# Kernel optimization log

Hardware: AMD Instinct MI355X
Metric: run time of the kernel (lower is better)

The kernel has to match this reference:

```python
import jax, jax.numpy as jnp
import numpy as np

N_NODES = 100000
N_EDGES = 2000000


def _init_mlp(key, dims, scale=0.05):
    Ws, bs = [], []
    ks = jax.random.split(key, len(dims) - 1)
    for k, di, do in zip(ks, dims[:-1], dims[1:]):
        Ws.append(jax.random.normal(k, (di, do), dtype=jnp.float32) * scale)
        bs.append(jnp.zeros((do,), dtype=jnp.float32))
    return Ws, bs


def setup_inputs() -> dict:
    key = jax.random.key(0)
    ks = jax.random.split(key, 7)
    d = {
        "t": jax.random.uniform(ks[0], (1,), dtype=jnp.float32),
        "x": jax.random.normal(ks[1], (N_NODES, 4), dtype=jnp.float32),
        "Ofixed": jax.random.normal(ks[2], (N_NODES, 2), dtype=jnp.float32),
        "src_idx": jax.random.randint(ks[3], (N_EDGES,), 0, N_NODES, dtype=jnp.int32),
        "tgt_idx": jax.random.randint(ks[4], (N_EDGES,), 0, N_NODES, dtype=jnp.int32),
    }
    # fR: (2*d_O+1)=13 -> [150]*4 -> 50 ; fO: 50 -> [100] -> 4
    R_Ws, R_bs = _init_mlp(ks[5], [13, 150, 150, 150, 150, 50])
    O_Ws, O_bs = _init_mlp(ks[6], [50, 100, 4])
    for i, (W, b) in enumerate(zip(R_Ws, R_bs)):
        d[f"fR_W{i}"] = W
        d[f"fR_b{i}"] = b
    for i, (W, b) in enumerate(zip(O_Ws, O_bs)):
        d[f"fO_W{i}"] = W
        d[f"fO_b{i}"] = b
    return d


def _mlp(h, Ws, bs):
    # hidden layers with ReLU, linear output (matches MLP in the torch code)
    for W, b in zip(Ws[:-1], bs[:-1]):
        h = jax.nn.relu(h @ W + b)
    return h @ Ws[-1] + bs[-1]


def reference(t, x, Ofixed, src_idx, tgt_idx,
              fR_W0, fR_b0, fR_W1, fR_b1, fR_W2, fR_b2, fR_W3, fR_b3, fR_W4, fR_b4,
              fO_W0, fO_b0, fO_W1, fO_b1):
    O = jnp.concatenate([x, Ofixed], axis=1)            # [N, d_O]
    # Msrc.T @ O and Mtgt.T @ O with 0/1 incidence matrices == gathers
    Rsrc = O[src_idx]                                   # [M, d_O]
    Rtgt = O[tgt_idx]                                   # [M, d_O]
    tt = jnp.broadcast_to(t.reshape(1, 1).astype(O.dtype), (src_idx.shape[0], 1))
    R_prime = jnp.concatenate([Rsrc, Rtgt, tt], axis=1)  # [M, 2*d_O+1]
    E = _mlp(R_prime, [fR_W0, fR_W1, fR_W2, fR_W3, fR_W4],
             [fR_b0, fR_b1, fR_b2, fR_b3, fR_b4])        # [M, d_E]
    # Mtgt @ E == scatter-add of edge messages onto target nodes
    E_prime = jax.ops.segment_sum(E, tgt_idx, num_segments=x.shape[0])  # [N, d_E]
    P = _mlp(E_prime, [fO_W0, fO_W1], [fO_b0, fO_b1])    # [N, d_P]
    return P
```

## Files before the change

kernel.cpp:

```cpp
#include <hip/hip_runtime.h>
#include <hip/hip_bf16.h>

typedef unsigned short u16;
typedef unsigned int u32;
typedef __attribute__((ext_vector_type(8))) short short8;
typedef __attribute__((ext_vector_type(4))) float f32x4;

constexpr int SA     = 192;
constexpr int BLK_E  = 128;
constexpr int NTHR   = 256;
constexpr int CHUNK  = 512;
constexpr int WSLOT  = 50 * CHUNK;
constexpr size_t WS_HDR   = 262144;

constexpr int Ls (int s) { return s == 0 ? 0 : (s <= 15 ? 1 + (s - 1) / 5 : 4); }
constexpr int Kss(int s) { return s == 0 ? 0 : (s <= 15 ? (s - 1) % 5 : s - 16); }

__device__ __forceinline__ int aswz(int row, int elem) {
    return row * SA + (elem ^ ((row & 7) << 3));
}

__device__ __forceinline__ u16 f2bf(float f) {
    union { float f; unsigned u; } c; c.f = f;
    return (u16)((c.u + 0x7fffu + ((c.u >> 16) & 1u)) >> 16);
}
__device__ __forceinline__ unsigned pk_bf16(float a, float b) {
    float2 f; f.x = a; f.y = b;
    __hip_bfloat162 h = __float22bfloat162_rn(f);
    return *(unsigned*)&h;
}

__device__ __forceinline__ int kperm(int kp) {
    if (kp < 64)  return (kp & 3) * 16 + (kp >> 2);
    if (kp < 128) { const int m = kp - 64; return (5 + (m & 3)) * 16 + (m >> 2); }
    if (kp < 144) return 4 * 16 + (kp - 128);
    if (kp < 160) return 9 * 16 + (kp - 144);
    return 1 << 30;
}

__global__ void prep_all(const float* __restrict__ W0, const float* __restrict__ W1,
                         const float* __restrict__ W2, const float* __restrict__ W3,
                         const float* __restrict__ W4,
                         const float* __restrict__ B0, const float* __restrict__ B1,
                         const float* __restrict__ B2, const float* __restrict__ B3,
                         const float* __restrict__ B4,
                         u16* __restrict__ Wt)
{
    const int l = blockIdx.y;
    const float* W; const float* B; int DI, DO; bool perm;
    if      (l == 0) { W = W0; B = B0; DI = 13;  DO = 150; perm = false; }
    else if (l == 1) { W = W1; B = B1; DI = 150; DO = 150; perm = true;  }
    else if (l == 2) { W = W2; B = B2; DI = 150; DO = 150; perm = true;  }
    else if (l == 3) { W = W3; B = B3; DI = 150; DO = 150; perm = true;  }
    else             { W = W4; B = B4; DI = 150; DO = 50;  perm = true;  }
    const int kbias = (l == 0) ? 13 : 150;
    u16* dst = Wt + (size_t)l * WSLOT;
    for (int idx = blockIdx.x * blockDim.x + threadIdx.x; idx < WSLOT;
         idx += gridDim.x * blockDim.x) {
        const int chunk = idx / CHUNK;
        const int within = idx - chunk * CHUNK;
        const int lane = within >> 3, e = within & 7;
        const int ks = chunk / 10, j = chunk - ks * 10;
        const int c = lane & 15, q = lane >> 4;
        const int n = j * 16 + c;
        const int kphys = ks * 32 + q * 8 + e;
        const int klog = perm ? kperm(kphys) : kphys;
        float v = 0.f;
        if (n < DO) {
            if (klog < DI)          v = W[klog * DO + n];
            else if (klog == kbias) v = B[n];
        }
        dst[idx] = f2bf(v);
    }
}

__device__ __forceinline__ void loadHalf(const u16* __restrict__ Wt,
                                         int l, int ks, int g, int nch,
                                         int lane, short8* buf)
{
    const u16* base = Wt + (size_t)l * WSLOT + (size_t)(ks * 10 + g * 5) * CHUNK
                         + lane * 8;
#pragma unroll
    for (int jj = 0; jj < 5; ++jj)
        if (jj < nch) buf[jj] = *(const short8*)&base[jj * CHUNK];
}

__device__ __forceinline__ void epilogueF(u16* act, int ebase, int col, int quad,
                                          f32x4 (&acc)[2][10])
{
#pragma unroll
    for (int mtl = 0; mtl < 2; ++mtl)
#pragma unroll
        for (int r = 0; r < 4; ++r) {
            const int row = ebase + mtl * 16 + quad * 4 + r;
            uint2 p0, p1;
            p0.x = pk_bf16(fmaxf(acc[mtl][0][r], 0.f), fmaxf(acc[mtl][1][r], 0.f));
            p0.y = pk_bf16(fmaxf(acc[mtl][2][r], 0.f), fmaxf(acc[mtl][3][r], 0.f));
            p1.x = pk_bf16(fmaxf(acc[mtl][5][r], 0.f), fmaxf(acc[mtl][6][r], 0.f));
            p1.y = pk_bf16(fmaxf(acc[mtl][7][r], 0.f), fmaxf(acc[mtl][8][r], 0.f));
            *(uint2*)&act[aswz(row, col * 4)]      = p0;
            *(uint2*)&act[aswz(row, 64 + col * 4)] = p1;
            act[aswz(row, 128 + col)] =
                (u16)pk_bf16(fmaxf(acc[mtl][4][r], 0.f), 0.f);
            u16 sv = (u16)pk_bf16(fmaxf(acc[mtl][9][r], 0.f), 0.f);
            if (col == 6) sv = 0x3F80;
            act[aswz(row, 144 + col)] = sv;
        }
}

__global__ void hist_kernel(const int* __restrict__ tgt, u32* __restrict__ cnt,
                            int n_edges)
{
    const int e = blockIdx.x * blockDim.x + threadIdx.x;
    if (e < n_edges) atomicAdd(&cnt[tgt[e]], 1u);
}

__global__ void scan1_kernel(const u32* __restrict__ cnt, u32* __restrict__ offs,
                             u32* __restrict__ bsum, int n)
{
    __shared__ u32 s[256];
    const int i = blockIdx.x * 256 + threadIdx.x;
    const u32 v = (i < n) ? cnt[i] : 0u;
    s[threadIdx.x] = v; __syncthreads();
#pragma unroll
    for (int d = 1; d < 256; d <<= 1) {
        const u32 t = (threadIdx.x >= d) ? s[threadIdx.x - d] : 0u;
        __syncthreads();
        s[threadIdx.x] += t;
        __syncthreads();
    }
    if (i < n) offs[i] = s[threadIdx.x] - v;
    if (threadIdx.x == 255) bsum[blockIdx.x] = s[255];
}

__global__ void scan2_kernel(u32* __restrict__ bsum, int nb)
{
    __shared__ u32 s[512];
    const int i = threadIdx.x;
    const u32 v = (i < nb) ? bsum[i] : 0u;
    s[i] = v; __syncthreads();
#pragma unroll
    for (int d = 1; d < 512; d <<= 1) {
        const u32 t = (i >= d) ? s[i - d] : 0u;
        __syncthreads();
        s[i] += t;
        __syncthreads();
    }
    if (i < nb) bsum[i] = s[i] - v;
}

__global__ void scan3_kernel(u32* __restrict__ offs, const u32* __restrict__ bsum,
                             u32* __restrict__ cursor, int n, int n_edges)
{
    const int i = blockIdx.x * 256 + threadIdx.x;
    if (i < n) {
        const u32 o = offs[i] + bsum[blockIdx.x];
        offs[i] = o;
        cursor[i] = o;
    }
    if (blockIdx.x == 0 && threadIdx.x == 0) offs[n] = (u32)n_edges;
}

__global__ void perm_kernel(const int* __restrict__ src, const int* __restrict__ tgt,
                            u32* __restrict__ cursor, int2* __restrict__ sg,
                            int n_edges)
{
    const int e = blockIdx.x * blockDim.x + threadIdx.x;
    if (e < n_edges) {
        const int g = tgt[e];
        const u32 pos = atomicAdd(&cursor[g], 1u);
        sg[pos] = make_int2(src[e], g);
    }
}

__global__ __launch_bounds__(NTHR, 3) void edge_kernel(
    const float* __restrict__ t, const float* __restrict__ x, const float* __restrict__ Ofx,
    const int2* __restrict__ sgp,
    const u16* __restrict__ Wt,
    float* __restrict__ Ep, int n_edges)
{
    __shared__ __align__(16) u16 act[BLK_E * SA];
    __shared__ int tgt_s[BLK_E];

    const int tid   = threadIdx.x;
    const int lane  = tid & 63;
    const int wv    = tid >> 6;
    const int ebase = wv * 32;
    const int col   = lane & 15;
    const int quad  = lane >> 4;

    if (lane < 32) {
        const int e = ebase + lane;
        const long long ge = (long long)blockIdx.x * BLK_E + e;
        const bool valid = ge < n_edges;
        const int2 sg = valid ? sgp[ge] : make_int2(0, 0);
        const int g = valid ? sg.y : -1;
        const float4 xs = valid ? *(const float4*)&x[(size_t)sg.x * 4] : float4{0, 0, 0, 0};
        const float2 os = valid ? *(const float2*)&Ofx[(size_t)sg.x * 2] : float2{0, 0};
        const float4 xg = valid ? *(const float4*)&x[(size_t)sg.y * 4] : float4{0, 0, 0, 0};
        const float2 og = valid ? *(const float2*)&Ofx[(size_t)sg.y * 2] : float2{0, 0};
        const float tv = valid ? t[0] : 0.f;
        uint4 w0, w1;
        w0.x = pk_bf16(xs.x, xs.y); w0.y = pk_bf16(xs.z, xs.w);
        w0.z = pk_bf16(os.x, os.y); w0.w = pk_bf16(xg.x, xg.y);
        w1.x = pk_bf16(xg.z, xg.w); w1.y = pk_bf16(og.x, og.y);
        w1.z = pk_bf16(tv, 1.0f);   w1.w = 0u;
        *(uint4*)&act[aswz(e, 0)]  = w0;
        *(uint4*)&act[aswz(e, 8)]  = w1;
        *(uint4*)&act[aswz(e, 16)] = uint4{0, 0, 0, 0};
        *(uint4*)&act[aswz(e, 24)] = uint4{0, 0, 0, 0};
        tgt_s[e] = g;
    }

    const f32x4 z = {0.f, 0.f, 0.f, 0.f};
    f32x4 acc[2][10];
    short8 Wb[2][5];
    short8 Af[2];

    loadHalf(Wt, 0, 0, 0, 5, lane, Wb[0]);
    loadHalf(Wt, 0, 0, 1, 5, lane, Wb[1]);

#pragma unroll
    for (int s = 0; s <= 15; ++s) {
        const int ks = Kss(s);
        const bool first = (s == 0) || (ks == 0);
#pragma unroll
        for (int mtl = 0; mtl < 2; ++mtl)
            Af[mtl] = *(const short8*)&act[aswz(ebase + mtl * 16 + col,
                                                ks * 32 + quad * 8)];
#pragma unroll
        for (int jj = 0; jj < 5; ++jj)
#pragma unroll
            for (int mtl = 0; mtl < 2; ++mtl)
                acc[mtl][jj] = __builtin_amdgcn_mfma_f32_16x16x32_bf16(
                    Af[mtl], Wb[0][jj], first ? z : acc[mtl][jj], 0, 0, 0);
        if (s < 15) loadHalf(Wt, Ls(s + 1), Kss(s + 1), 0, 5, lane, Wb[0]);
        else        loadHalf(Wt, 4, 0, 0, 4, lane, Wb[0]);
#pragma unroll
        for (int jj = 0; jj < 5; ++jj)
#pragma unroll
            for (int mtl = 0; mtl < 2; ++mtl)
                acc[mtl][5 + jj] = __builtin_amdgcn_mfma_f32_16x16x32_bf16(
                    Af[mtl], Wb[1][jj], first ? z : acc[mtl][5 + jj], 0, 0, 0);
        if (s < 15) loadHalf(Wt, Ls(s + 1), Kss(s + 1), 1, 5, lane, Wb[1]);
        else        loadHalf(Wt, 4, 1, 0, 4, lane, Wb[1]);
        if (s == 0 || ks == 4)
            epilogueF(act, ebase, col, quad, acc);
    }

    f32x4 acc4[2][4];
#pragma unroll
    for (int ks = 0; ks < 5; ++ks) {
#pragma unroll
        for (int mtl = 0; mtl < 2; ++mtl)
            Af[mtl] = *(const short8*)&act[aswz(ebase + mtl * 16 + col,
                                                ks * 32 + quad * 8)];
#pragma unroll
        for (int jj = 0; jj < 4; ++jj)
#pragma unroll
            for (int mtl = 0; mtl < 2; ++mtl)
                acc4[mtl][jj] = __builtin_amdgcn_mfma_f32_16x16x32_bf16(
                    Af[mtl], Wb[ks & 1][jj], (ks == 0) ? z : acc4[mtl][jj], 0, 0, 0);
        if (ks + 2 <= 4) loadHalf(Wt, 4, ks + 2, 0, 4, lane, Wb[ks & 1]);
    }

    float* actF = (float*)&act[ebase * SA];
#pragma unroll
    for (int mtl = 0; mtl < 2; ++mtl)
#pragma unroll
        for (int jj = 0; jj < 4; ++jj) {
            const int n = jj * 16 + col;
            if (n < 50) {
#pragma unroll
                for (int r = 0; r < 4; ++r)
                    actF[(mtl * 16 + quad * 4 + r) * 52 + n] = acc4[mtl][jj][r];
            }
        }
    if (lane < 50) {
        const int c = lane;
        int   cur = tgt_s[ebase];
        float a   = 0.f;
        for (int r = 0; r < 32; ++r) {
            const int   g = tgt_s[ebase + r];
            const float v = actF[r * 52 + c];
            if (g != cur) {
                if (cur >= 0) atomicAdd(&Ep[(size_t)cur * 50 + c], a);
                a = 0.f; cur = g;
            }
            a += v;
        }
        if (cur >= 0) atomicAdd(&Ep[(size_t)cur * 50 + c], a);
    }
}

template<int DI, int DO, bool RELU>
__device__ __forceinline__ void mlp_layer_t(
    const float* __restrict__ W, const float* __restrict__ B,
    float (*in)[64], float (*out)[64], int tid)
{
    const int et = tid & 15;
    const int jt = tid >> 4;
    constexpr int NG = (DO + 15) / 16;

    float acc0[NG], acc1[NG], acc2[NG], acc3[NG];
#pragma unroll
    for (int g = 0; g < NG; ++g) {
        const int j = jt + 16 * g;
        const float bb = (j < DO) ? B[j] : 0.f;
        acc0[g] = bb; acc1[g] = bb; acc2[g] = bb; acc3[g] = bb;
    }
    for (int k = 0; k < DI; ++k) {
        const float4 a = *(const float4*)&in[k][et * 4];
#pragma unroll
        for (int g = 0; g < NG; ++g) {
            const int j = jt + 16 * g;
            const float wv = (j < DO) ? W[k * DO + j] : 0.f;
            acc0[g] = fmaf(a.x, wv, acc0[g]);
            acc1[g] = fmaf(a.y, wv, acc1[g]);
            acc2[g] = fmaf(a.z, wv, acc2[g]);
            acc3[g] = fmaf(a.w, wv, acc3[g]);
        }
    }
#pragma unroll
    for (int g = 0; g < NG; ++g) {
        const int j = jt + 16 * g;
        if (j < DO) {
            float4 v; v.x = acc0[g]; v.y = acc1[g]; v.z = acc2[g]; v.w = acc3[g];
            if (RELU) {
                v.x = fmaxf(v.x, 0.f); v.y = fmaxf(v.y, 0.f);
                v.z = fmaxf(v.z, 0.f); v.w = fmaxf(v.w, 0.f);
            }
            *(float4*)&out[j][et * 4] = v;
        }
    }
}

__global__ __launch_bounds__(256, 2) void node_kernel(
    const float* __restrict__ Ep,
    const float* __restrict__ W0, const float* __restrict__ B0,
    const float* __restrict__ W1, const float* __restrict__ B1,
    float* __restrict__ P, int n_nodes)
{
    __shared__ float bufA[104][64];
    __shared__ float bufB[104][64];
    const int tid = threadIdx.x;
    const int n0  = blockIdx.x * 64;

    for (int idx = tid; idx < 64 * 50; idx += 256) {
        const int e = idx / 50;
        const int k = idx - e * 50;
        const int n = n0 + e;
        bufA[k][e] = (n < n_nodes) ? Ep[(size_t)n * 50 + k] : 0.f;
    }
    __syncthreads();
    mlp_layer_t<50, 100, true >(W0, B0, bufA, bufB, tid); __syncthreads();
    mlp_layer_t<100, 4, false>(W1, B1, bufB, bufA, tid); __syncthreads();
    for (int idx = tid; idx < 64 * 4; idx += 256) {
        const int e = idx & 63;
        const int j = idx >> 6;
        const int n = n0 + e;
        if (n < n_nodes) P[(size_t)n * 4 + j] = bufA[j][e];
    }
}

extern "C" void kernel_launch(void* const* d_in, const int* in_sizes, int n_in,
                              void* d_out, int out_size, void* d_ws, size_t ws_size,
                              hipStream_t stream)
{
    const float* t   = (const float*)d_in[0];
    const float* x   = (const float*)d_in[1];
    const float* Ofx = (const float*)d_in[2];
    const int*   src = (const int*)d_in[3];
    const int*   tgt = (const int*)d_in[4];
    const float* W0  = (const float*)d_in[5];  const float* B0 = (const float*)d_in[6];
    const float* W1  = (const float*)d_in[7];  const float* B1 = (const float*)d_in[8];
    const float* W2  = (const float*)d_in[9];  const float* B2 = (const float*)d_in[10];
    const float* W3  = (const float*)d_in[11]; const float* B3 = (const float*)d_in[12];
    const float* W4  = (const float*)d_in[13]; const float* B4 = (const float*)d_in[14];
    const float* OW0 = (const float*)d_in[15]; const float* OB0 = (const float*)d_in[16];
    const float* OW1 = (const float*)d_in[17]; const float* OB1 = (const float*)d_in[18];

    const int n_nodes = in_sizes[1] / 4;
    const int n_edges = in_sizes[3];

    auto align256 = [](size_t v) { return (v + 255) & ~(size_t)255; };
    char* ws = (char*)d_ws;
    const size_t copy_elems = (size_t)n_nodes * 50;
    size_t o = 0;
    u16*   Wt       = (u16*)(ws + o);  o = WS_HDR;
    float* Ep       = (float*)(ws + o); o = align256(o + copy_elems * sizeof(float));
    u32*   offs     = (u32*)(ws + o);  o = align256(o + (size_t)(n_nodes + 1) * 4);
    u32*   cursor   = (u32*)(ws + o);  o = align256(o + (size_t)n_nodes * 4);
    u32*   bsum     = (u32*)(ws + o);  o = align256(o + 512 * 4);
    int2*  sg_perm  = (int2*)(ws + o); o = align256(o + (size_t)n_edges * 8);

    const int NB  = (n_nodes + 255) / 256;
    const int EBK = (n_edges + 255) / 256;

    prep_all<<<dim3(32, 5), 256, 0, stream>>>(W0, W1, W2, W3, W4,
                                              B0, B1, B2, B3, B4, Wt);
    hipMemsetAsync(Ep, 0, copy_elems * sizeof(float), stream);
    hipMemsetAsync(cursor, 0, (size_t)n_nodes * 4, stream);

    hist_kernel <<<EBK, 256, 0, stream>>>(tgt, cursor, n_edges);
    scan1_kernel<<<NB, 256, 0, stream>>>(cursor, offs, bsum, n_nodes);
    scan2_kernel<<<1, 512, 0, stream>>>(bsum, NB);
    scan3_kernel<<<NB, 256, 0, stream>>>(offs, bsum, cursor, n_nodes, n_edges);
    perm_kernel <<<EBK, 256, 0, stream>>>(src, tgt, cursor, sg_perm, n_edges);

    edge_kernel<<<(n_edges + BLK_E - 1) / BLK_E, NTHR, 0, stream>>>(
        t, x, Ofx, sg_perm, Wt, Ep, n_edges);

    node_kernel<<<(n_nodes + 63) / 64, 256, 0, stream>>>(
        Ep, OW0, OB0, OW1, OB1, (float*)d_out, n_nodes);
}
```

Before: 884.9 us.

## Triple-buffer weight fragments in edge MLP and fold cursor memset into prep

The edge kernel's weight register buffering goes from two half-tiles to three, so each half-tile is loaded three steps ahead of its MFMA use instead of two, which should hide more global/L2 load latency. A unified half index function replaces the per-step layer and k-step arithmetic. Separately, zeroing the cursor array moves into an extra blockIdx.y slice of prep_all, which drops one memset launch. The third buffer costs 40 more VGPRs per thread and may lower occupancy or cause spills.

```diff
diff --git a/kernel.cpp b/kernel.cpp
--- a/kernel.cpp
+++ b/kernel.cpp
@@ -44,9 +44,15 @@
                          const float* __restrict__ B0, const float* __restrict__ B1,
                          const float* __restrict__ B2, const float* __restrict__ B3,
                          const float* __restrict__ B4,
-                         u16* __restrict__ Wt)
+                         u16* __restrict__ Wt, u32* __restrict__ cursor, int n_nodes)
 {
     const int l = blockIdx.y;
+    if (l == 5) {
+        for (int idx = blockIdx.x * blockDim.x + threadIdx.x; idx < n_nodes;
+             idx += gridDim.x * blockDim.x)
+            cursor[idx] = 0u;
+        return;
+    }
     const float* W; const float* B; int DI, DO; bool perm;
     if      (l == 0) { W = W0; B = B0; DI = 13;  DO = 150; perm = false; }
     else if (l == 1) { W = W1; B = B1; DI = 150; DO = 150; perm = true;  }
@@ -74,10 +80,12 @@
     }
 }
 
-__device__ __forceinline__ void loadHalf(const u16* __restrict__ Wt,
-                                         int l, int ks, int g, int nch,
-                                         int lane, short8* buf)
-{
+__device__ __forceinline__ void loadHalfH(const u16* __restrict__ Wt, int h,
+                                          int lane, short8* buf)
+{
+    int l, ks, g, nch;
+    if (h < 32) { const int s = h >> 1; l = Ls(s); ks = Kss(s); g = h & 1; nch = 5; }
+    else        { l = 4; ks = h - 32; g = 0; nch = 4; }
     const u16* base = Wt + (size_t)l * WSLOT + (size_t)(ks * 10 + g * 5) * CHUNK
                          + lane * 8;
 #pragma unroll
@@ -214,16 +222,18 @@
 
     const f32x4 z = {0.f, 0.f, 0.f, 0.f};
     f32x4 acc[2][10];
-    short8 Wb[2][5];
+    short8 Wb[3][5];
     short8 Af[2];
 
-    loadHalf(Wt, 0, 0, 0, 5, lane, Wb[0]);
-    loadHalf(Wt, 0, 0, 1, 5, lane, Wb[1]);
+    loadHalfH(Wt, 0, lane, Wb[0]);
+    loadHalfH(Wt, 1, lane, Wb[1]);
+    loadHalfH(Wt, 2, lane, Wb[2]);
 
 #pragma unroll
     for (int s = 0; s <= 15; ++s) {
         const int ks = Kss(s);
         const bool first = (s == 0) || (ks == 0);
+        const int h0 = 2 * s, h1 = 2 * s + 1;
 #pragma unroll
         for (int mtl = 0; mtl < 2; ++mtl)
             Af[mtl] = *(const short8*)&act[aswz(ebase + mtl * 16 + col,
@@ -233,35 +243,34 @@
 #pragma unroll
             for (int mtl = 0; mtl < 2; ++mtl)
                 acc[mtl][jj] = __builtin_amdgcn_mfma_f32_16x16x32_bf16(
-                    Af[mtl], Wb[0][jj], first ? z : acc[mtl][jj], 0, 0, 0);
-        if (s < 15) loadHalf(Wt, Ls(s + 1), Kss(s + 1), 0, 5, lane, Wb[0]);
-        else        loadHalf(Wt, 4, 0, 0, 4, lane, Wb[0]);
+                    Af[mtl], Wb[h0 % 3][jj], first ? z : acc[mtl][jj], 0, 0, 0);
+        loadHalfH(Wt, h0 + 3, lane, Wb[h0 % 3]);
 #pragma unroll
         for (int jj = 0; jj < 5; ++jj)
 #pragma unroll
             for (int mtl = 0; mtl < 2; ++mtl)
                 acc[mtl][5 + jj] = __builtin_amdgcn_mfma_f32_16x16x32_bf16(
-                    Af[mtl], Wb[1][jj], first ? z : acc[mtl][5 + jj], 0, 0, 0);
-        if (s < 15) loadHalf(Wt, Ls(s + 1), Kss(s + 1), 1, 5, lane, Wb[1]);
-        else        loadHalf(Wt, 4, 1, 0, 4, lane, Wb[1]);
+                    Af[mtl], Wb[h1 % 3][jj], first ? z : acc[mtl][5 + jj], 0, 0, 0);
+        loadHalfH(Wt, h1 + 3, lane, Wb[h1 % 3]);
         if (s == 0 || ks == 4)
             epilogueF(act, ebase, col, quad, acc);
     }
 
     f32x4 acc4[2][4];
 #pragma unroll
-    for (int ks = 0; ks < 5; ++ks) {
+    for (int ks4 = 0; ks4 < 5; ++ks4) {
+        const int h = 32 + ks4;
 #pragma unroll
         for (int mtl = 0; mtl < 2; ++mtl)
             Af[mtl] = *(const short8*)&act[aswz(ebase + mtl * 16 + col,
-                                                ks * 32 + quad * 8)];
+                                                ks4 * 32 + quad * 8)];
 #pragma unroll
         for (int jj = 0; jj < 4; ++jj)
 #pragma unroll
             for (int mtl = 0; mtl < 2; ++mtl)
                 acc4[mtl][jj] = __builtin_amdgcn_mfma_f32_16x16x32_bf16(
-                    Af[mtl], Wb[ks & 1][jj], (ks == 0) ? z : acc4[mtl][jj], 0, 0, 0);
-        if (ks + 2 <= 4) loadHalf(Wt, 4, ks + 2, 0, 4, lane, Wb[ks & 1]);
+                    Af[mtl], Wb[h % 3][jj], (ks4 == 0) ? z : acc4[mtl][jj], 0, 0, 0);
+        if (h + 3 <= 36) loadHalfH(Wt, h + 3, lane, Wb[h % 3]);
     }
 
     float* actF = (float*)&act[ebase * SA];
@@ -397,10 +406,10 @@
     const int NB  = (n_nodes + 255) / 256;
     const int EBK = (n_edges + 255) / 256;
 
-    prep_all<<<dim3(32, 5), 256, 0, stream>>>(W0, W1, W2, W3, W4,
-                                              B0, B1, B2, B3, B4, Wt);
+    prep_all<<<dim3(32, 6), 256, 0, stream>>>(W0, W1, W2, W3, W4,
+                                              B0, B1, B2, B3, B4, Wt,
+                                              cursor, n_nodes);
     hipMemsetAsync(Ep, 0, copy_elems * sizeof(float), stream);
-    hipMemsetAsync(cursor, 0, (size_t)n_nodes * 4, stream);
 
     hist_kernel <<<EBK, 256, 0, stream>>>(tgt, cursor, n_edges);
     scan1_kernel<<<NB, 256, 0, stream>>>(cursor, offs, bsum, n_nodes);
```

Measured after the change: 870.6 us. No clear change (-1.6%).
